# Performance work log

Measured on AMD Instinct MI355X. Metric: run time of the kernel, lower is better.

## Reference

```python
import jax, jax.numpy as jnp
import numpy as np


def setup_inputs() -> dict:
    key = jax.random.key(0)
    ks = jax.random.split(key, 6)
    B, S, D = 2, 2048, 1024
    E, DFF = 8, 2048  # E includes always-on expert 0; router sees E-1 routed experts
    scale = 0.02
    return {
        "hidden_states": jax.random.normal(ks[0], (B, S, D), dtype=jnp.float32),
        "router_w": jax.random.normal(ks[1], (D, E - 1), dtype=jnp.float32) * scale,
        "router_b": jnp.zeros((E - 1,), dtype=jnp.float32),
        "wg": jax.random.normal(ks[2], (E, D, DFF), dtype=jnp.float32) * scale,
        "wu": jax.random.normal(ks[3], (E, D, DFF), dtype=jnp.float32) * scale,
        "wd": jax.random.normal(ks[4], (E, DFF, D), dtype=jnp.float32) * scale,
        "top_k": 2,
    }


def _expert_mlp(x, wg_e, wu_e, wd_e):
    # SwiGLU MLP: down( silu(x @ gate) * (x @ up) )
    return (jax.nn.silu(x @ wg_e) * (x @ wu_e)) @ wd_e


def reference(hidden_states, router_w, router_b, wg, wu, wd, top_k):
    B, S, D = hidden_states.shape
    E = wg.shape[0]  # total experts incl. always-on expert 0
    x = hidden_states.reshape(-1, D)  # [T, D]
    T = x.shape[0]

    # Router over E-1 routed experts, softmax in float32
    router_logits = x @ router_w + router_b  # [T, E-1]
    probs = jax.nn.softmax(router_logits.astype(jnp.float32), axis=-1)
    topw, topi = jax.lax.top_k(probs, top_k)  # [T, k]
    topw = topw / jnp.sum(topw, axis=-1, keepdims=True)
    topw = topw.astype(x.dtype)

    # Dense combine weights over routed experts (0 for unselected)
    cw = jnp.zeros((T, E - 1), dtype=x.dtype)
    cw = cw.at[jnp.arange(T)[:, None], topi].add(topw)  # [T, E-1]

    # Always-on expert 0 with weight 1
    out = _expert_mlp(x, wg[0], wu[0], wd[0])  # [T, D]

    # Routed experts 1..E-1 (static small loop over experts)
    for e in range(1, E):
        ye = _expert_mlp(x, wg[e], wu[e], wd[e])  # [T, D]
        out = out + cw[:, e - 1, None] * ye

    return out.reshape(B, S, -1)
```

## Files before the change

### kernel.cpp

```cpp
#include <hip/hip_runtime.h>

#define T_TOK 4096
#define DIM   1024
#define DFF   2048
#define NE    8
#define NR    7
#define MAXNB 71
#define NY    (32 + MAXNB)
#define G_BUF 20480

typedef __bf16 bf16x8 __attribute__((ext_vector_type(8)));
typedef float  floatx4 __attribute__((ext_vector_type(4)));

__device__ __forceinline__ unsigned short f32_bf16(float f) {
  union { float f; unsigned int u; } v; v.f = f;
  unsigned int u = v.u;
  unsigned int r = (u + 0x7FFFu + ((u >> 16) & 1u)) >> 16;
  return (unsigned short)r;
}

typedef __attribute__((address_space(3))) void lds_void_t;
typedef const __attribute__((address_space(1))) void g_void_t;

__device__ __forceinline__ void gld16(const void* g, void* l) {
  __builtin_amdgcn_global_load_lds((g_void_t*)g, (lds_void_t*)l, 16, 0, 0);
}

__global__ __launch_bounds__(256) void cvt_x_kernel(const float4* __restrict__ in,
                                                    ushort4* __restrict__ out) {
  int i = blockIdx.x * 256 + threadIdx.x;
  float4 v = in[i];
  ushort4 o;
  o.x = f32_bf16(v.x); o.y = f32_bf16(v.y);
  o.z = f32_bf16(v.z); o.w = f32_bf16(v.w);
  out[i] = o;
}

__global__ __launch_bounds__(256) void router_kernel(const float* __restrict__ x,
                                                     const float* __restrict__ rw,
                                                     const float* __restrict__ rb,
                                                     int* __restrict__ idxR,
                                                     float* __restrict__ wslR,
                                                     int* __restrict__ cnt,
                                                     int4* __restrict__ tokE,
                                                     float2* __restrict__ tokW) {
  const int lane = threadIdx.x & 63;
  const int t = blockIdx.x * 4 + (threadIdx.x >> 6);
  const float* xr = x + (size_t)t * DIM;
  float acc[NR];
#pragma unroll
  for (int e = 0; e < NR; e++) acc[e] = 0.f;
  for (int d = lane; d < DIM; d += 64) {
    float xv = xr[d];
#pragma unroll
    for (int e = 0; e < NR; e++) acc[e] += xv * rw[d * NR + e];
  }
#pragma unroll
  for (int off = 32; off > 0; off >>= 1) {
#pragma unroll
    for (int e = 0; e < NR; e++) acc[e] += __shfl_xor(acc[e], off, 64);
  }
  if (lane == 0) {
    float lg[NR];
    float m = -1e30f;
#pragma unroll
    for (int e = 0; e < NR; e++) { lg[e] = acc[e] + rb[e]; m = fmaxf(m, lg[e]); }
    float p[NR], s = 0.f;
#pragma unroll
    for (int e = 0; e < NR; e++) { p[e] = expf(lg[e] - m); s += p[e]; }
#pragma unroll
    for (int e = 0; e < NR; e++) p[e] /= s;
    int i1 = 0;
#pragma unroll
    for (int e = 1; e < NR; e++) if (p[e] > p[i1]) i1 = e;
    int i2 = (i1 == 0) ? 1 : 0;
#pragma unroll
    for (int e = 0; e < NR; e++) if (e != i1 && p[e] > p[i2]) i2 = e;
    float w1 = p[i1], w2 = p[i2], sw = w1 + w2;
    float w1n = w1 / sw, w2n = w2 / sw;
    int s1 = atomicAdd(&cnt[i1], 1);
    idxR[i1 * 4096 + s1] = t; wslR[i1 * 4096 + s1] = w1n;
    int s2 = atomicAdd(&cnt[i2], 1);
    idxR[i2 * 4096 + s2] = t; wslR[i2 * 4096 + s2] = w2n;
    int4 te; te.x = i1; te.y = s1; te.z = i2; te.w = s2;
    tokE[t] = te;
    float2 tw; tw.x = w1n; tw.y = w2n;
    tokW[t] = tw;
  }
}

__global__ __launch_bounds__(256) void sched_kernel(const int* __restrict__ cnt,
                                                    int* __restrict__ idxR,
                                                    float* __restrict__ wslR,
                                                    int4* __restrict__ schedAll,
                                                    int4* __restrict__ schedP,
                                                    int* __restrict__ prefOut,
                                                    int rsb) {
  __shared__ int nb[NR], pref[NR];
  if (threadIdx.x == 0) {
    int p = 0;
    for (int e = 0; e < NR; e++) { int c = cnt[e]; int n = (c + 127) >> 7; nb[e] = n; pref[e] = p; p += n; }
  }
  __syncthreads();
  if (threadIdx.x < NR) prefOut[threadIdx.x] = pref[threadIdx.x];
  for (int e = 0; e < NR; e++) {
    int c = cnt[e], top = nb[e] * 128;
    for (int i = c + (int)threadIdx.x; i < top; i += 256) {
      idxR[e * 4096 + i] = 0; wslR[e * 4096 + i] = 0.f;
    }
  }
  const int NBtot = pref[NR - 1] + nb[NR - 1];
  for (int y = threadIdx.x; y < 32; y += 256) {
    int4 ent; ent.x = 0; ent.y = -1; ent.z = y * 128; ent.w = 0;
    schedAll[y] = ent;
  }
  for (int y = threadIdx.x; y < MAXNB; y += 256) {
    int4 ent; ent.x = -1; ent.y = 0; ent.z = 0; ent.w = 0;
    if (y < NBtot) {
#pragma unroll
      for (int e = 0; e < NR; e++)
        if (y >= pref[e] && y < pref[e] + nb[e]) {
          int rb2 = y - pref[e];
          ent.x = e + 1; ent.y = e * 4096 + rb2 * 128; ent.z = rsb + y * 128;
        }
    }
    schedAll[32 + y] = ent;
  }
  for (int i = threadIdx.x; i < NR * 32; i += 256) {
    int e = i >> 5, rb2 = i & 31;
    int4 ent; ent.w = 0;
    if (rb2 < nb[e]) { ent.x = e + 1; ent.y = e * 4096 + rb2 * 128; ent.z = rb2 * 128; }
    else             { ent.x = -1; ent.y = 0; ent.z = 0; }
    schedP[i] = ent;
  }
}

__global__ __launch_bounds__(256) void transpose_cvt_kernel(
    const float* __restrict__ wg, const float* __restrict__ wu, const float* __restrict__ wd,
    unsigned short* __restrict__ wgt, unsigned short* __restrict__ wut,
    unsigned short* __restrict__ wdt) {
  __shared__ float tile[64][65];
  const int z = blockIdx.z;
  const float* src; unsigned short* dst; int R, C;
  if (z < 8)       { src = wg + (size_t)z * DIM * DFF;        dst = wgt + (size_t)z * DIM * DFF;        R = DIM; C = DFF; }
  else if (z < 16) { src = wu + (size_t)(z - 8) * DIM * DFF;  dst = wut + (size_t)(z - 8) * DIM * DFF;  R = DIM; C = DFF; }
  else             { src = wd + (size_t)(z - 16) * DFF * DIM; dst = wdt + (size_t)(z - 16) * DFF * DIM; R = DFF; C = DIM; }
  const int c0 = blockIdx.x * 64, r0 = blockIdx.y * 64;
  if (c0 >= C || r0 >= R) return;
  const int tx = threadIdx.x & 63, ty = threadIdx.x >> 6;
#pragma unroll
  for (int j = ty; j < 64; j += 4)
    tile[j][tx] = src[(size_t)(r0 + j) * C + c0 + tx];
  __syncthreads();
  const int r2 = (threadIdx.x & 15) * 4, jj = threadIdx.x >> 4;
#pragma unroll
  for (int j = jj; j < 64; j += 16) {
    unsigned int lo = (unsigned int)f32_bf16(tile[r2 + 0][j]) | ((unsigned int)f32_bf16(tile[r2 + 1][j]) << 16);
    unsigned int hi = (unsigned int)f32_bf16(tile[r2 + 2][j]) | ((unsigned int)f32_bf16(tile[r2 + 3][j]) << 16);
    uint2 o; o.x = lo; o.y = hi;
    *(uint2*)(dst + (size_t)(c0 + j) * R + r0 + r2) = o;
  }
}

__global__ __launch_bounds__(512, 2) void gemm1_kernel(
    const unsigned short* __restrict__ xb, const unsigned short* __restrict__ wgt,
    const unsigned short* __restrict__ wut, const int* __restrict__ idxR,
    const int4* __restrict__ sched, unsigned short* __restrict__ h, int gy) {
  const int nblk = gridDim.x;
  int bid = blockIdx.x;
  { int q = nblk >> 3, r = nblk & 7, xc = bid & 7, p = bid >> 3;
    bid = (xc < r ? xc * (q + 1) : r * (q + 1) + (xc - r) * q) + p; }
  const int bx = bid / gy, by = bid - bx * gy;
  const int4 ent = sched[by];
  if (ent.x < 0) return;
  __shared__ unsigned short smem[3 * G_BUF];
  const int tid = threadIdx.x, lane = tid & 63, wid = tid >> 6;
  const int n0 = bx * 256;
  const int wm = (wid >> 2) * 64;
  const int wn = (wid & 3) * 64;
  const int fr = lane & 15, kq = lane >> 4;
  const int pl = (fr >> 1) * 64 + (((((fr & 1) << 2) | kq) ^ (fr >> 1)) << 3);
  int offA[4], offG[4], offU[4];
#pragma unroll
  for (int mi = 0; mi < 4; mi++) offA[mi] = (wm + mi * 16) * 32 + pl;
#pragma unroll
  for (int ni = 0; ni < 4; ni++) {
    offG[ni] = 4096 + (wn + ni * 16) * 32 + pl;
    offU[ni] = 12288 + (wn + ni * 16) * 32 + pl;
  }
  const int prA = tid >> 3;
  const int csA = (tid & 7) ^ (prA & 7);
  const int rowS = 2 * prA + (csA >> 2);
  const int colS = (csA & 3) * 8;
  int tokA;
  if (ent.y < 0) tokA = ent.z + rowS;
  else           tokA = idxR[ent.y + rowS];
  const unsigned short* wgt_e = wgt + (size_t)ent.x * DIM * DFF;
  const unsigned short* wut_e = wut + (size_t)ent.x * DIM * DFF;
  const unsigned short* gA  = xb + (size_t)tokA * DIM + colS;
  const unsigned short* gG0 = wgt_e + (size_t)(n0 + rowS) * DIM + colS;
  const unsigned short* gG1 = gG0 + (size_t)128 * DIM;
  const unsigned short* gU0 = wut_e + (size_t)(n0 + rowS) * DIM + colS;
  const unsigned short* gU1 = gU0 + (size_t)128 * DIM;
  floatx4 accg[4][4], accu[4][4];
  const floatx4 z4 = {0.f, 0.f, 0.f, 0.f};
#pragma unroll
  for (int i = 0; i < 4; i++)
#pragma unroll
    for (int j = 0; j < 4; j++) { accg[i][j] = z4; accu[i][j] = z4; }
  {
    unsigned short* d = smem + tid * 8;
    gld16(gA, d); gld16(gG0, d + 4096); gld16(gG1, d + 8192);
    gld16(gU0, d + 12288); gld16(gU1, d + 16384);
    unsigned short* e = smem + G_BUF + tid * 8;
    gld16(gA + 32, e); gld16(gG0 + 32, e + 4096); gld16(gG1 + 32, e + 8192);
    gld16(gU0 + 32, e + 12288); gld16(gU1 + 32, e + 16384);
  }
  asm volatile("s_waitcnt vmcnt(5)" ::: "memory");
  __builtin_amdgcn_s_barrier();
  int b = 0;
  for (int k = 0; k < 32; ++k) {
    const unsigned short* Bb = smem + b * G_BUF;
    int b2 = b + 2; if (b2 >= 3) b2 -= 3;
    unsigned short* db2 = smem + b2 * G_BUF + tid * 8;
    if (k < 30) {
      const int kt = (k + 2) * 32;
      gld16(gA + kt, db2); gld16(gG0 + kt, db2 + 4096); gld16(gG1 + kt, db2 + 8192);
      gld16(gU0 + kt, db2 + 12288); gld16(gU1 + kt, db2 + 16384);
    }
    __builtin_amdgcn_sched_barrier(0);
    bf16x8 a[4], g[4], u[4];
#pragma unroll
    for (int mi = 0; mi < 4; mi++) a[mi] = *(const bf16x8*)(Bb + offA[mi]);
#pragma unroll
    for (int ni = 0; ni < 4; ni++) {
      g[ni] = *(const bf16x8*)(Bb + offG[ni]);
      u[ni] = *(const bf16x8*)(Bb + offU[ni]);
    }
    __builtin_amdgcn_s_setprio(1);
#pragma unroll
    for (int mi = 0; mi < 4; mi++)
#pragma unroll
      for (int ni = 0; ni < 4; ni++)
        accg[mi][ni] = __builtin_amdgcn_mfma_f32_16x16x32_bf16(a[mi], g[ni], accg[mi][ni], 0, 0, 0);
#pragma unroll
    for (int mi = 0; mi < 4; mi++)
#pragma unroll
      for (int ni = 0; ni < 4; ni++)
        accu[mi][ni] = __builtin_amdgcn_mfma_f32_16x16x32_bf16(a[mi], u[ni], accu[mi][ni], 0, 0, 0);
    __builtin_amdgcn_s_setprio(0);
    __builtin_amdgcn_sched_barrier(0);
    if (k < 30)       asm volatile("s_waitcnt vmcnt(5)" ::: "memory");
    else if (k == 30) asm volatile("s_waitcnt vmcnt(0)" ::: "memory");
    __builtin_amdgcn_s_barrier();
    b++; if (b == 3) b = 0;
  }
  const int rb = kq * 4;
#pragma unroll
  for (int mi = 0; mi < 4; mi++)
#pragma unroll
    for (int ni = 0; ni < 4; ni++)
#pragma unroll
      for (int r = 0; r < 4; r++) {
        int row = ent.z + wm + mi * 16 + rb + r;
        int col = n0 + wn + ni * 16 + fr;
        float gv = accg[mi][ni][r], uv = accu[mi][ni][r];
        float hv = (gv / (1.f + __expf(-gv))) * uv;
        h[(size_t)row * DFF + col] = f32_bf16(hv);
      }
}

__global__ __launch_bounds__(512, 2) void gemm2_kernel(
    const unsigned short* __restrict__ hsrc, const unsigned short* __restrict__ wdt,
    const int4* __restrict__ sched, float* __restrict__ y, int gy) {
  const int nblk = gridDim.x;
  int bid = blockIdx.x;
  { int q = nblk >> 3, r = nblk & 7, xc = bid & 7, p = bid >> 3;
    bid = (xc < r ? xc * (q + 1) : r * (q + 1) + (xc - r) * q) + p; }
  const int bx = bid / gy, by = bid - bx * gy;
  const int4 ent = sched[by];
  if (ent.x < 0) return;
  __shared__ unsigned short smem[3 * G_BUF];
  const int tid = threadIdx.x, lane = tid & 63, wid = tid >> 6;
  const int n0 = bx * 512;
  const int wm = (wid >> 2) * 64;
  const int wn = (wid & 3) * 128;
  const int fr = lane & 15, kq = lane >> 4;
  const int pl = (fr >> 1) * 64 + (((((fr & 1) << 2) | kq) ^ (fr >> 1)) << 3);
  int offA[4], offB[8];
#pragma unroll
  for (int mi = 0; mi < 4; mi++) offA[mi] = (wm + mi * 16) * 32 + pl;
#pragma unroll
  for (int ni = 0; ni < 8; ni++) offB[ni] = 4096 + (wn + ni * 16) * 32 + pl;
  const int prA = tid >> 3;
  const int csA = (tid & 7) ^ (prA & 7);
  const int rowS = 2 * prA + (csA >> 2);
  const int colS = (csA & 3) * 8;
  const unsigned short* wdt_e = wdt + (size_t)ent.x * DFF * DIM;
  const unsigned short* gA  = hsrc + (size_t)(ent.z + rowS) * DFF + colS;
  const unsigned short* gB0 = wdt_e + (size_t)(n0 + rowS) * DFF + colS;
  const unsigned short* gB1 = gB0 + (size_t)128 * DFF;
  const unsigned short* gB2 = gB0 + (size_t)256 * DFF;
  const unsigned short* gB3 = gB0 + (size_t)384 * DFF;
  floatx4 acc[4][8];
  const floatx4 z4 = {0.f, 0.f, 0.f, 0.f};
#pragma unroll
  for (int i = 0; i < 4; i++)
#pragma unroll
    for (int j = 0; j < 8; j++) acc[i][j] = z4;
  {
    unsigned short* d = smem + tid * 8;
    gld16(gA, d); gld16(gB0, d + 4096); gld16(gB1, d + 8192);
    gld16(gB2, d + 12288); gld16(gB3, d + 16384);
    unsigned short* e = smem + G_BUF + tid * 8;
    gld16(gA + 32, e); gld16(gB0 + 32, e + 4096); gld16(gB1 + 32, e + 8192);
    gld16(gB2 + 32, e + 12288); gld16(gB3 + 32, e + 16384);
  }
  asm volatile("s_waitcnt vmcnt(5)" ::: "memory");
  __builtin_amdgcn_s_barrier();
  int b = 0;
  for (int k = 0; k < 64; ++k) {
    const unsigned short* Bb = smem + b * G_BUF;
    int b2 = b + 2; if (b2 >= 3) b2 -= 3;
    unsigned short* db2 = smem + b2 * G_BUF + tid * 8;
    if (k < 62) {
      const int kt = (k + 2) * 32;
      gld16(gA + kt, db2); gld16(gB0 + kt, db2 + 4096); gld16(gB1 + kt, db2 + 8192);
      gld16(gB2 + kt, db2 + 12288); gld16(gB3 + kt, db2 + 16384);
    }
    __builtin_amdgcn_sched_barrier(0);
    bf16x8 a[4], bf[8];
#pragma unroll
    for (int mi = 0; mi < 4; mi++) a[mi] = *(const bf16x8*)(Bb + offA[mi]);
#pragma unroll
    for (int ni = 0; ni < 8; ni++) bf[ni] = *(const bf16x8*)(Bb + offB[ni]);
    __builtin_amdgcn_s_setprio(1);
#pragma unroll
    for (int mi = 0; mi < 4; mi++)
#pragma unroll
      for (int ni = 0; ni < 8; ni++)
        acc[mi][ni] = __builtin_amdgcn_mfma_f32_16x16x32_bf16(a[mi], bf[ni], acc[mi][ni], 0, 0, 0);
    __builtin_amdgcn_s_setprio(0);
    __builtin_amdgcn_sched_barrier(0);
    if (k < 62)       asm volatile("s_waitcnt vmcnt(5)" ::: "memory");
    else if (k == 62) asm volatile("s_waitcnt vmcnt(0)" ::: "memory");
    __builtin_amdgcn_s_barrier();
    b++; if (b == 3) b = 0;
  }
  const int rb = kq * 4;
#pragma unroll
  for (int mi = 0; mi < 4; mi++)
#pragma unroll
    for (int ni = 0; ni < 8; ni++)
#pragma unroll
      for (int r = 0; r < 4; r++)
        y[(size_t)(ent.z + wm + mi * 16 + rb + r) * DIM + n0 + wn + ni * 16 + fr] = acc[mi][ni][r];
}

__global__ __launch_bounds__(256) void gemm2_atomic_kernel(
    const unsigned short* __restrict__ h, const unsigned short* __restrict__ wdt,
    const int* __restrict__ idxR, const float* __restrict__ wslR,
    const int4* __restrict__ sched, float* __restrict__ out) {
  const int4 ent = sched[blockIdx.y];
  if (ent.x < 0) return;
  __shared__ unsigned short As[128 * 32];
  __shared__ unsigned short Bs[128 * 32];
  const int tid = threadIdx.x, lane = tid & 63, wid = tid >> 6;
  const int n0 = blockIdx.x * 128;
  const int wm = (wid >> 1) * 64, wn = (wid & 1) * 64;
  floatx4 acc[4][4];
  const floatx4 z4 = {0.f, 0.f, 0.f, 0.f};
#pragma unroll
  for (int i = 0; i < 4; i++)
#pragma unroll
    for (int j = 0; j < 4; j++) acc[i][j] = z4;
  const unsigned short* wdt_e = wdt + (size_t)ent.x * DFF * DIM;
  const int srow = tid >> 2, scol = (tid & 3) * 8;
  const unsigned short* ap0 = h + (size_t)(ent.z + srow) * DFF + scol;
  const unsigned short* ap1 = ap0 + (size_t)64 * DFF;
  const unsigned short* bp0 = wdt_e + (size_t)(n0 + srow) * DFF + scol;
  const unsigned short* bp1 = bp0 + (size_t)64 * DFF;
  unsigned short* as0 = As + tid * 8;
  unsigned short* as1 = As + (256 + tid) * 8;
  unsigned short* bs0 = Bs + tid * 8;
  unsigned short* bs1 = Bs + (256 + tid) * 8;
  const int fr = lane & 15, kq = (lane >> 4) * 8;
  for (int k0 = 0; k0 < DFF; k0 += 32) {
    __syncthreads();
    gld16(ap0 + k0, as0); gld16(ap1 + k0, as1);
    gld16(bp0 + k0, bs0); gld16(bp1 + k0, bs1);
    __syncthreads();
    bf16x8 af[4], bf[4];
#pragma unroll
    for (int mi = 0; mi < 4; mi++) af[mi] = *(const bf16x8*)(As + (wm + mi * 16 + fr) * 32 + kq);
#pragma unroll
    for (int ni = 0; ni < 4; ni++) bf[ni] = *(const bf16x8*)(Bs + (wn + ni * 16 + fr) * 32 + kq);
#pragma unroll
    for (int mi = 0; mi < 4; mi++)
#pragma unroll
      for (int ni = 0; ni < 4; ni++)
        acc[mi][ni] = __builtin_amdgcn_mfma_f32_16x16x32_bf16(af[mi], bf[ni], acc[mi][ni], 0, 0, 0);
  }
  const int rb0 = wm + (lane >> 4) * 4;
  const int cb0 = n0 + wn + fr;
#pragma unroll
  for (int mi = 0; mi < 4; mi++)
#pragma unroll
    for (int r = 0; r < 4; r++) {
      int lrow = rb0 + mi * 16 + r;
      if (ent.y < 0) {
        int tok = ent.z + lrow;
#pragma unroll
        for (int ni = 0; ni < 4; ni++)
          out[(size_t)tok * DIM + cb0 + ni * 16] = acc[mi][ni][r];
      } else {
        int tok = idxR[ent.y + lrow];
        float s = wslR[ent.y + lrow];
        if (s != 0.f) {
#pragma unroll
          for (int ni = 0; ni < 4; ni++)
            atomicAdd(&out[(size_t)tok * DIM + cb0 + ni * 16], s * acc[mi][ni][r]);
        }
      }
    }
}

__global__ __launch_bounds__(256) void combine_kernel(const float* __restrict__ y,
                                                      const int4* __restrict__ tokE,
                                                      const float2* __restrict__ tokW,
                                                      const int* __restrict__ pref,
                                                      float* __restrict__ out) {
  const int t = blockIdx.x;
  const int c = threadIdx.x * 4;
  int4 te = tokE[t];
  float2 tw = tokW[t];
  int p1 = 4096 + pref[te.x] * 128 + te.y;
  int p2 = 4096 + pref[te.z] * 128 + te.w;
  float4 a = *(const float4*)(y + (size_t)t * DIM + c);
  float4 b = *(const float4*)(y + (size_t)p1 * DIM + c);
  float4 d = *(const float4*)(y + (size_t)p2 * DIM + c);
  float4 o;
  o.x = a.x + tw.x * b.x + tw.y * d.x;
  o.y = a.y + tw.x * b.y + tw.y * d.y;
  o.z = a.z + tw.x * b.z + tw.y * d.z;
  o.w = a.w + tw.x * b.w + tw.y * d.w;
  *(float4*)(out + (size_t)t * DIM + c) = o;
}

extern "C" void kernel_launch(void* const* d_in, const int* in_sizes, int n_in,
                              void* d_out, int out_size, void* d_ws, size_t ws_size,
                              hipStream_t stream) {
  const float* x  = (const float*)d_in[0];
  const float* rw = (const float*)d_in[1];
  const float* rb = (const float*)d_in[2];
  const float* wg = (const float*)d_in[3];
  const float* wu = (const float*)d_in[4];
  const float* wd = (const float*)d_in[5];
  float* out = (float*)d_out;

  const bool modeA = ws_size >= (size_t)163300000;
  const bool modeB = !modeA && ws_size >= (size_t)146700000;
  const size_t H_ROWS = modeA ? 13184 : (modeB ? 9088 : 4096);
  const int rsb = modeA ? 4096 : 0;

  char* p = (char*)d_ws;
  unsigned short* xb  = (unsigned short*)p; p += (size_t)T_TOK * DIM * 2;
  unsigned short* h   = (unsigned short*)p; p += H_ROWS * DFF * 2;
  unsigned short* wgt = (unsigned short*)p;
  float*          y   = (float*)p;          p += (size_t)NE * DIM * DFF * 2;
  unsigned short* wut = (unsigned short*)p; p += (size_t)NE * DIM * DFF * 2;
  unsigned short* wdt = (unsigned short*)p; p += (size_t)NE * DIM * DFF * 2;
  int*   idxR = (int*)p;   p += (size_t)NR * 4096 * 4;
  float* wslR;
  if (modeA) { wslR = (float*)wdt; }
  else       { wslR = (float*)p; p += (size_t)NR * 4096 * 4; }
  int*   cnt  = (int*)p;      p += 64;
  int*   pref = (int*)p;      p += 64;
  int4*  schedAll = (int4*)p; p += 2048;
  int4*  schedP   = (int4*)p; p += 4096;
  int4*  tokE = (int4*)p;     p += (size_t)T_TOK * 16;
  float2* tokW = (float2*)p;  p += (size_t)T_TOK * 8;

  cvt_x_kernel<<<dim3(T_TOK * DIM / 4 / 256), 256, 0, stream>>>((const float4*)x, (ushort4*)xb);
  hipMemsetAsync(cnt, 0, 64, stream);
  router_kernel<<<dim3(T_TOK / 4), 256, 0, stream>>>(x, rw, rb, idxR, wslR, cnt, tokE, tokW);
  sched_kernel<<<dim3(1), 256, 0, stream>>>(cnt, idxR, wslR, schedAll, schedP, pref, rsb);
  transpose_cvt_kernel<<<dim3(32, 32, 24), 256, 0, stream>>>(wg, wu, wd, wgt, wut, wdt);

  if (modeA) {
    gemm1_kernel<<<dim3((DFF / 256) * NY), 512, 0, stream>>>(xb, wgt, wut, idxR, schedAll, h, NY);
    gemm2_kernel<<<dim3((DIM / 512) * NY), 512, 0, stream>>>(h, wdt, schedAll, y, NY);
    combine_kernel<<<dim3(T_TOK), 256, 0, stream>>>(y, tokE, tokW, pref, out);
  } else if (modeB) {
    gemm1_kernel<<<dim3((DFF / 256) * 32), 512, 0, stream>>>(xb, wgt, wut, idxR, schedAll, h, 32);
    gemm2_atomic_kernel<<<dim3(DIM / 128, 32), 256, 0, stream>>>(h, wdt, idxR, wslR, schedAll, out);
    gemm1_kernel<<<dim3((DFF / 256) * MAXNB), 512, 0, stream>>>(xb, wgt, wut, idxR, schedAll + 32, h, MAXNB);
    gemm2_atomic_kernel<<<dim3(DIM / 128, MAXNB), 256, 0, stream>>>(h, wdt, idxR, wslR, schedAll + 32, out);
  } else {
    gemm1_kernel<<<dim3((DFF / 256) * 32), 512, 0, stream>>>(xb, wgt, wut, idxR, schedAll, h, 32);
    gemm2_atomic_kernel<<<dim3(DIM / 128, 32), 256, 0, stream>>>(h, wdt, idxR, wslR, schedAll, out);
    for (int e = 0; e < NR; e++) {
      gemm1_kernel<<<dim3((DFF / 256) * 32), 512, 0, stream>>>(xb, wgt, wut, idxR, schedP + e * 32, h, 32);
      gemm2_atomic_kernel<<<dim3(DIM / 128, 32), 256, 0, stream>>>(h, wdt, idxR, wslR, schedP + e * 32, out);
    }
  }
}
```

Baseline: 568.5 us.

## Re-tile grouped GEMMs into two-phase ping-pong with split gate/up warps

Both grouped GEMM kernels now give each warp the full 128-row M slice (8 MFMA row tiles) and a 64-wide N slice. In gemm1, the low four warps compute the gate product and the high four compute the up product, and the up accumulators are passed through LDS for the SiLU epilogue. Each K step is split into two halves, with barriers and global-load issue placed between the MFMA bursts, so that LDS reads, async copies and matrix math interleave across warps. The change adds barriers and an LDS exchange epilogue, and it changes register pressure, in exchange for less redundant LDS fragment traffic and better overlap.

```diff
diff --git a/kernel.cpp b/kernel.cpp
--- a/kernel.cpp
+++ b/kernel.cpp
@@ -176,18 +176,15 @@
   __shared__ unsigned short smem[3 * G_BUF];
   const int tid = threadIdx.x, lane = tid & 63, wid = tid >> 6;
   const int n0 = bx * 256;
-  const int wm = (wid >> 2) * 64;
   const int wn = (wid & 3) * 64;
   const int fr = lane & 15, kq = lane >> 4;
   const int pl = (fr >> 1) * 64 + (((((fr & 1) << 2) | kq) ^ (fr >> 1)) << 3);
-  int offA[4], offG[4], offU[4];
-#pragma unroll
-  for (int mi = 0; mi < 4; mi++) offA[mi] = (wm + mi * 16) * 32 + pl;
-#pragma unroll
-  for (int ni = 0; ni < 4; ni++) {
-    offG[ni] = 4096 + (wn + ni * 16) * 32 + pl;
-    offU[ni] = 12288 + (wn + ni * 16) * 32 + pl;
-  }
+  int offA[8], offB[4];
+#pragma unroll
+  for (int mi = 0; mi < 8; mi++) offA[mi] = mi * 512 + pl;
+  const int bsec = (wid < 4) ? 4096 : 12288;
+#pragma unroll
+  for (int ni = 0; ni < 4; ni++) offB[ni] = bsec + (wn + ni * 16) * 32 + pl;
   const int prA = tid >> 3;
   const int csA = (tid & 7) ^ (prA & 7);
   const int rowS = 2 * prA + (csA >> 2);
@@ -202,12 +199,12 @@
   const unsigned short* gG1 = gG0 + (size_t)128 * DIM;
   const unsigned short* gU0 = wut_e + (size_t)(n0 + rowS) * DIM + colS;
   const unsigned short* gU1 = gU0 + (size_t)128 * DIM;
-  floatx4 accg[4][4], accu[4][4];
+  floatx4 acc[8][4];
   const floatx4 z4 = {0.f, 0.f, 0.f, 0.f};
 #pragma unroll
-  for (int i = 0; i < 4; i++)
-#pragma unroll
-    for (int j = 0; j < 4; j++) { accg[i][j] = z4; accu[i][j] = z4; }
+  for (int i = 0; i < 8; i++)
+#pragma unroll
+    for (int j = 0; j < 4; j++) acc[i][j] = z4;
   {
     unsigned short* d = smem + tid * 8;
     gld16(gA, d); gld16(gG0, d + 4096); gld16(gG1, d + 8192);
@@ -219,55 +216,82 @@
   asm volatile("s_waitcnt vmcnt(5)" ::: "memory");
   __builtin_amdgcn_s_barrier();
   int b = 0;
+  bf16x8 a[8], bf[4];
   for (int k = 0; k < 32; ++k) {
     const unsigned short* Bb = smem + b * G_BUF;
     int b2 = b + 2; if (b2 >= 3) b2 -= 3;
     unsigned short* db2 = smem + b2 * G_BUF + tid * 8;
-    if (k < 30) {
-      const int kt = (k + 2) * 32;
-      gld16(gA + kt, db2); gld16(gG0 + kt, db2 + 4096); gld16(gG1 + kt, db2 + 8192);
-      gld16(gU0 + kt, db2 + 12288); gld16(gU1 + kt, db2 + 16384);
+    const bool pf = (k < 30);
+    const int kt = (k + 2) * 32;
+#pragma unroll
+    for (int mi = 0; mi < 4; mi++) a[mi] = *(const bf16x8*)(Bb + offA[mi]);
+#pragma unroll
+    for (int ni = 0; ni < 4; ni++) bf[ni] = *(const bf16x8*)(Bb + offB[ni]);
+    if (pf) { gld16(gA + kt, db2); gld16(gG0 + kt, db2 + 4096); gld16(gG1 + kt, db2 + 8192); }
+    __builtin_amdgcn_sched_barrier(0);
+    __builtin_amdgcn_s_barrier();
+    asm volatile("s_waitcnt lgkmcnt(0)" ::: "memory");
+    __builtin_amdgcn_sched_barrier(0);
+    __builtin_amdgcn_s_setprio(1);
+#pragma unroll
+    for (int mi = 0; mi < 4; mi++)
+#pragma unroll
+      for (int ni = 0; ni < 4; ni++)
+        acc[mi][ni] = __builtin_amdgcn_mfma_f32_16x16x32_bf16(a[mi], bf[ni], acc[mi][ni], 0, 0, 0);
+    __builtin_amdgcn_s_setprio(0);
+    __builtin_amdgcn_sched_barrier(0);
+    __builtin_amdgcn_s_barrier();
+#pragma unroll
+    for (int mi = 4; mi < 8; mi++) a[mi] = *(const bf16x8*)(Bb + offA[mi]);
+    if (pf) { gld16(gU0 + kt, db2 + 12288); gld16(gU1 + kt, db2 + 16384); }
+    __builtin_amdgcn_sched_barrier(0);
+    __builtin_amdgcn_s_barrier();
+    asm volatile("s_waitcnt lgkmcnt(0)" ::: "memory");
+    __builtin_amdgcn_sched_barrier(0);
+    __builtin_amdgcn_s_setprio(1);
+#pragma unroll
+    for (int mi = 4; mi < 8; mi++)
+#pragma unroll
+      for (int ni = 0; ni < 4; ni++)
+        acc[mi][ni] = __builtin_amdgcn_mfma_f32_16x16x32_bf16(a[mi], bf[ni], acc[mi][ni], 0, 0, 0);
+    __builtin_amdgcn_s_setprio(0);
+    __builtin_amdgcn_sched_barrier(0);
+    if (pf)           asm volatile("s_waitcnt vmcnt(5)" ::: "memory");
+    else if (k == 30) asm volatile("s_waitcnt vmcnt(0)" ::: "memory");
+    __builtin_amdgcn_s_barrier();
+    b++; if (b == 3) b = 0;
+  }
+  float* xch = (float*)smem;
+  const int xbase = (wid & 3) * (64 * 67) + lane * 67;
+#pragma unroll
+  for (int chunk = 0; chunk < 2; ++chunk) {
+    __syncthreads();
+    if (wid >= 4) {
+#pragma unroll
+      for (int mi = 0; mi < 4; mi++)
+#pragma unroll
+        for (int ni = 0; ni < 4; ni++)
+#pragma unroll
+          for (int r = 0; r < 4; r++)
+            xch[xbase + mi * 16 + ni * 4 + r] = acc[chunk * 4 + mi][ni][r];
     }
-    __builtin_amdgcn_sched_barrier(0);
-    bf16x8 a[4], g[4], u[4];
-#pragma unroll
-    for (int mi = 0; mi < 4; mi++) a[mi] = *(const bf16x8*)(Bb + offA[mi]);
-#pragma unroll
-    for (int ni = 0; ni < 4; ni++) {
-      g[ni] = *(const bf16x8*)(Bb + offG[ni]);
-      u[ni] = *(const bf16x8*)(Bb + offU[ni]);
+    __syncthreads();
+    if (wid < 4) {
+#pragma unroll
+      for (int mi = 0; mi < 4; mi++)
+#pragma unroll
+        for (int ni = 0; ni < 4; ni++)
+#pragma unroll
+          for (int r = 0; r < 4; r++) {
+            float gv = acc[chunk * 4 + mi][ni][r];
+            float uv = xch[xbase + mi * 16 + ni * 4 + r];
+            float hv = (gv / (1.f + __expf(-gv))) * uv;
+            int row = ent.z + (chunk * 4 + mi) * 16 + kq * 4 + r;
+            int col = n0 + wn + ni * 16 + fr;
+            h[(size_t)row * DFF + col] = f32_bf16(hv);
+          }
     }
-    __builtin_amdgcn_s_setprio(1);
-#pragma unroll
-    for (int mi = 0; mi < 4; mi++)
-#pragma unroll
-      for (int ni = 0; ni < 4; ni++)
-        accg[mi][ni] = __builtin_amdgcn_mfma_f32_16x16x32_bf16(a[mi], g[ni], accg[mi][ni], 0, 0, 0);
-#pragma unroll
-    for (int mi = 0; mi < 4; mi++)
-#pragma unroll
-      for (int ni = 0; ni < 4; ni++)
-        accu[mi][ni] = __builtin_amdgcn_mfma_f32_16x16x32_bf16(a[mi], u[ni], accu[mi][ni], 0, 0, 0);
-    __builtin_amdgcn_s_setprio(0);
-    __builtin_amdgcn_sched_barrier(0);
-    if (k < 30)       asm volatile("s_waitcnt vmcnt(5)" ::: "memory");
-    else if (k == 30) asm volatile("s_waitcnt vmcnt(0)" ::: "memory");
-    __builtin_amdgcn_s_barrier();
-    b++; if (b == 3) b = 0;
-  }
-  const int rb = kq * 4;
-#pragma unroll
-  for (int mi = 0; mi < 4; mi++)
-#pragma unroll
-    for (int ni = 0; ni < 4; ni++)
-#pragma unroll
-      for (int r = 0; r < 4; r++) {
-        int row = ent.z + wm + mi * 16 + rb + r;
-        int col = n0 + wn + ni * 16 + fr;
-        float gv = accg[mi][ni][r], uv = accu[mi][ni][r];
-        float hv = (gv / (1.f + __expf(-gv))) * uv;
-        h[(size_t)row * DFF + col] = f32_bf16(hv);
-      }
+  }
 }
 
 __global__ __launch_bounds__(512, 2) void gemm2_kernel(
@@ -283,15 +307,14 @@
   __shared__ unsigned short smem[3 * G_BUF];
   const int tid = threadIdx.x, lane = tid & 63, wid = tid >> 6;
   const int n0 = bx * 512;
-  const int wm = (wid >> 2) * 64;
-  const int wn = (wid & 3) * 128;
+  const int wn = wid * 64;
   const int fr = lane & 15, kq = lane >> 4;
   const int pl = (fr >> 1) * 64 + (((((fr & 1) << 2) | kq) ^ (fr >> 1)) << 3);
-  int offA[4], offB[8];
-#pragma unroll
-  for (int mi = 0; mi < 4; mi++) offA[mi] = (wm + mi * 16) * 32 + pl;
-#pragma unroll
-  for (int ni = 0; ni < 8; ni++) offB[ni] = 4096 + (wn + ni * 16) * 32 + pl;
+  int offA[8], offB[4];
+#pragma unroll
+  for (int mi = 0; mi < 8; mi++) offA[mi] = mi * 512 + pl;
+#pragma unroll
+  for (int ni = 0; ni < 4; ni++) offB[ni] = 4096 + (wn + ni * 16) * 32 + pl;
   const int prA = tid >> 3;
   const int csA = (tid & 7) ^ (prA & 7);
   const int rowS = 2 * prA + (csA >> 2);
@@ -302,12 +325,12 @@
   const unsigned short* gB1 = gB0 + (size_t)128 * DFF;
   const unsigned short* gB2 = gB0 + (size_t)256 * DFF;
   const unsigned short* gB3 = gB0 + (size_t)384 * DFF;
-  floatx4 acc[4][8];
+  floatx4 acc[8][4];
   const floatx4 z4 = {0.f, 0.f, 0.f, 0.f};
 #pragma unroll
-  for (int i = 0; i < 4; i++)
-#pragma unroll
-    for (int j = 0; j < 8; j++) acc[i][j] = z4;
+  for (int i = 0; i < 8; i++)
+#pragma unroll
+    for (int j = 0; j < 4; j++) acc[i][j] = z4;
   {
     unsigned short* d = smem + tid * 8;
     gld16(gA, d); gld16(gB0, d + 4096); gld16(gB1, d + 8192);
@@ -319,42 +342,59 @@
   asm volatile("s_waitcnt vmcnt(5)" ::: "memory");
   __builtin_amdgcn_s_barrier();
   int b = 0;
+  bf16x8 a[8], bf[4];
   for (int k = 0; k < 64; ++k) {
     const unsigned short* Bb = smem + b * G_BUF;
     int b2 = b + 2; if (b2 >= 3) b2 -= 3;
     unsigned short* db2 = smem + b2 * G_BUF + tid * 8;
-    if (k < 62) {
-      const int kt = (k + 2) * 32;
-      gld16(gA + kt, db2); gld16(gB0 + kt, db2 + 4096); gld16(gB1 + kt, db2 + 8192);
-      gld16(gB2 + kt, db2 + 12288); gld16(gB3 + kt, db2 + 16384);
-    }
-    __builtin_amdgcn_sched_barrier(0);
-    bf16x8 a[4], bf[8];
+    const bool pf = (k < 62);
+    const int kt = (k + 2) * 32;
 #pragma unroll
     for (int mi = 0; mi < 4; mi++) a[mi] = *(const bf16x8*)(Bb + offA[mi]);
 #pragma unroll
-    for (int ni = 0; ni < 8; ni++) bf[ni] = *(const bf16x8*)(Bb + offB[ni]);
+    for (int ni = 0; ni < 4; ni++) bf[ni] = *(const bf16x8*)(Bb + offB[ni]);
+    if (pf) { gld16(gA + kt, db2); gld16(gB0 + kt, db2 + 4096); gld16(gB1 + kt, db2 + 8192); }
+    __builtin_amdgcn_sched_barrier(0);
+    __builtin_amdgcn_s_barrier();
+    asm volatile("s_waitcnt lgkmcnt(0)" ::: "memory");
+    __builtin_amdgcn_sched_barrier(0);
     __builtin_amdgcn_s_setprio(1);
 #pragma unroll
     for (int mi = 0; mi < 4; mi++)
 #pragma unroll
-      for (int ni = 0; ni < 8; ni++)
+      for (int ni = 0; ni < 4; ni++)
         acc[mi][ni] = __builtin_amdgcn_mfma_f32_16x16x32_bf16(a[mi], bf[ni], acc[mi][ni], 0, 0, 0);
     __builtin_amdgcn_s_setprio(0);
     __builtin_amdgcn_sched_barrier(0);
-    if (k < 62)       asm volatile("s_waitcnt vmcnt(5)" ::: "memory");
+    __builtin_amdgcn_s_barrier();
+#pragma unroll
+    for (int mi = 4; mi < 8; mi++) a[mi] = *(const bf16x8*)(Bb + offA[mi]);
+    if (pf) { gld16(gB2 + kt, db2 + 12288); gld16(gB3 + kt, db2 + 16384); }
+    __builtin_amdgcn_sched_barrier(0);
+    __builtin_amdgcn_s_barrier();
+    asm volatile("s_waitcnt lgkmcnt(0)" ::: "memory");
+    __builtin_amdgcn_sched_barrier(0);
+    __builtin_amdgcn_s_setprio(1);
+#pragma unroll
+    for (int mi = 4; mi < 8; mi++)
+#pragma unroll
+      for (int ni = 0; ni < 4; ni++)
+        acc[mi][ni] = __builtin_amdgcn_mfma_f32_16x16x32_bf16(a[mi], bf[ni], acc[mi][ni], 0, 0, 0);
+    __builtin_amdgcn_s_setprio(0);
+    __builtin_amdgcn_sched_barrier(0);
+    if (pf)           asm volatile("s_waitcnt vmcnt(5)" ::: "memory");
     else if (k == 62) asm volatile("s_waitcnt vmcnt(0)" ::: "memory");
     __builtin_amdgcn_s_barrier();
     b++; if (b == 3) b = 0;
   }
   const int rb = kq * 4;
 #pragma unroll
-  for (int mi = 0; mi < 4; mi++)
-#pragma unroll
-    for (int ni = 0; ni < 8; ni++)
+  for (int mi = 0; mi < 8; mi++)
+#pragma unroll
+    for (int ni = 0; ni < 4; ni++)
 #pragma unroll
       for (int r = 0; r < 4; r++)
-        y[(size_t)(ent.z + wm + mi * 16 + rb + r) * DIM + n0 + wn + ni * 16 + fr] = acc[mi][ni][r];
+        y[(size_t)(ent.z + mi * 16 + rb + r) * DIM + n0 + wn + ni * 16 + fr] = acc[mi][ni][r];
 }
 
 __global__ __launch_bounds__(256) void gemm2_atomic_kernel(
@@ -390,16 +430,16 @@
     gld16(ap0 + k0, as0); gld16(ap1 + k0, as1);
     gld16(bp0 + k0, bs0); gld16(bp1 + k0, bs1);
     __syncthreads();
-    bf16x8 af[4], bf[4];
+    bf16x8 af[4], bfv[4];
 #pragma unroll
     for (int mi = 0; mi < 4; mi++) af[mi] = *(const bf16x8*)(As + (wm + mi * 16 + fr) * 32 + kq);
 #pragma unroll
-    for (int ni = 0; ni < 4; ni++) bf[ni] = *(const bf16x8*)(Bs + (wn + ni * 16 + fr) * 32 + kq);
+    for (int ni = 0; ni < 4; ni++) bfv[ni] = *(const bf16x8*)(Bs + (wn + ni * 16 + fr) * 32 + kq);
 #pragma unroll
     for (int mi = 0; mi < 4; mi++)
 #pragma unroll
       for (int ni = 0; ni < 4; ni++)
-        acc[mi][ni] = __builtin_amdgcn_mfma_f32_16x16x32_bf16(af[mi], bf[ni], acc[mi][ni], 0, 0, 0);
+        acc[mi][ni] = __builtin_amdgcn_mfma_f32_16x16x32_bf16(af[mi], bfv[ni], acc[mi][ni], 0, 0, 0);
   }
   const int rb0 = wm + (lane >> 4) * 4;
   const int cb0 = n0 + wn + fr;
```

New measurement: 577.5 us. Within noise of the previous version (+1.6%).

## Load A operand directly to registers and split gate/up across wave groups

Applied to the files above, without the earlier changes.

Both GEMM kernels stop staging the A tile (activations) through LDS and instead load each wave's A fragments straight from global memory into registers, double-buffered across k-steps. In gemm1 the warp layout changes so half the waves compute the gate projection and half the up projection over a wider N tile, with the results exchanged through LDS in the epilogue to apply SiLU·up. This cuts LDS footprint and LDS read traffic per k-step, but makes A loads redundant across waves (served from cache) and adds an LDS exchange plus barriers in the gemm1 epilogue.

```diff
diff --git a/kernel.cpp b/kernel.cpp
--- a/kernel.cpp
+++ b/kernel.cpp
@@ -7,7 +7,7 @@
 #define NR    7
 #define MAXNB 71
 #define NY    (32 + MAXNB)
-#define G_BUF 20480
+#define BUFU  16384
 
 typedef __bf16 bf16x8 __attribute__((ext_vector_type(8)));
 typedef float  floatx4 __attribute__((ext_vector_type(4)));
@@ -162,6 +162,40 @@
   }
 }
 
+#define G1_TILE(KX, CUR, NXT)                                                            \
+  {                                                                                      \
+    const int k_ = (KX);                                                                 \
+    if (k_ < 31) {                                                                       \
+      _Pragma("unroll")                                                                  \
+      for (int mi = 0; mi < 4; mi++)                                                     \
+        NXT[mi] = *(const bf16x8*)(aP[mi] + (k_ + 1) * 32);                              \
+    }                                                                                    \
+    __builtin_amdgcn_sched_barrier(0);                                                   \
+    if (k_ < 30) {                                                                       \
+      const int kt_ = (k_ + 2) * 32;                                                     \
+      unsigned short* d_ = smem + b2_ * BUFU + tid * 8;                                  \
+      gld16(gG0 + kt_, d_);        gld16(gG1 + kt_, d_ + 4096);                          \
+      gld16(gU0 + kt_, d_ + 8192); gld16(gU1 + kt_, d_ + 12288);                         \
+    }                                                                                    \
+    __builtin_amdgcn_sched_barrier(0);                                                   \
+    const unsigned short* Bb_ = smem + b_ * BUFU + secB;                                 \
+    bf16x8 bf[8];                                                                        \
+    _Pragma("unroll")                                                                    \
+    for (int nb = 0; nb < 8; nb++) bf[nb] = *(const bf16x8*)(Bb_ + offB[nb]);            \
+    __builtin_amdgcn_s_setprio(1);                                                       \
+    _Pragma("unroll")                                                                    \
+    for (int mi = 0; mi < 4; mi++)                                                       \
+      _Pragma("unroll")                                                                  \
+      for (int nb = 0; nb < 8; nb++)                                                     \
+        acc[mi][nb] = __builtin_amdgcn_mfma_f32_16x16x32_bf16(CUR[mi], bf[nb], acc[mi][nb], 0, 0, 0); \
+    __builtin_amdgcn_s_setprio(0);                                                       \
+    __builtin_amdgcn_sched_barrier(0);                                                   \
+    if (k_ < 30)       asm volatile("s_waitcnt vmcnt(4)" ::: "memory");                  \
+    else if (k_ == 30) asm volatile("s_waitcnt vmcnt(0)" ::: "memory");                  \
+    __builtin_amdgcn_s_barrier();                                                        \
+    b_ = (b_ == 2) ? 0 : b_ + 1;  b2_ = (b2_ == 2) ? 0 : b2_ + 1;                        \
+  }
+
 __global__ __launch_bounds__(512, 2) void gemm1_kernel(
     const unsigned short* __restrict__ xb, const unsigned short* __restrict__ wgt,
     const unsigned short* __restrict__ wut, const int* __restrict__ idxR,
@@ -173,102 +207,127 @@
   const int bx = bid / gy, by = bid - bx * gy;
   const int4 ent = sched[by];
   if (ent.x < 0) return;
-  __shared__ unsigned short smem[3 * G_BUF];
+  __shared__ unsigned short smem[3 * BUFU];
   const int tid = threadIdx.x, lane = tid & 63, wid = tid >> 6;
   const int n0 = bx * 256;
-  const int wm = (wid >> 2) * 64;
-  const int wn = (wid & 3) * 64;
+  const int wm = (wid & 1) * 64;
+  const int wn = ((wid >> 1) & 1) * 128;
+  const bool isU = (wid >= 4);
+  const int secB = isU ? 8192 : 0;
   const int fr = lane & 15, kq = lane >> 4;
   const int pl = (fr >> 1) * 64 + (((((fr & 1) << 2) | kq) ^ (fr >> 1)) << 3);
-  int offA[4], offG[4], offU[4];
-#pragma unroll
-  for (int mi = 0; mi < 4; mi++) offA[mi] = (wm + mi * 16) * 32 + pl;
-#pragma unroll
-  for (int ni = 0; ni < 4; ni++) {
-    offG[ni] = 4096 + (wn + ni * 16) * 32 + pl;
-    offU[ni] = 12288 + (wn + ni * 16) * 32 + pl;
-  }
-  const int prA = tid >> 3;
-  const int csA = (tid & 7) ^ (prA & 7);
-  const int rowS = 2 * prA + (csA >> 2);
-  const int colS = (csA & 3) * 8;
-  int tokA;
-  if (ent.y < 0) tokA = ent.z + rowS;
-  else           tokA = idxR[ent.y + rowS];
+  int offB[8];
+#pragma unroll
+  for (int nb = 0; nb < 8; nb++) offB[nb] = (wn + nb * 16) * 32 + pl;
+  const unsigned short* aP[4];
+#pragma unroll
+  for (int mi = 0; mi < 4; mi++) {
+    int row = wm + mi * 16 + fr;
+    int tok = (ent.y < 0) ? (ent.z + row) : idxR[ent.y + row];
+    aP[mi] = xb + (size_t)tok * DIM + kq * 8;
+  }
+  const int pr = tid >> 3;
+  const int cs = (tid & 7) ^ (pr & 7);
+  const int rowS = 2 * pr + (cs >> 2);
+  const int colS = (cs & 3) * 8;
   const unsigned short* wgt_e = wgt + (size_t)ent.x * DIM * DFF;
   const unsigned short* wut_e = wut + (size_t)ent.x * DIM * DFF;
-  const unsigned short* gA  = xb + (size_t)tokA * DIM + colS;
   const unsigned short* gG0 = wgt_e + (size_t)(n0 + rowS) * DIM + colS;
   const unsigned short* gG1 = gG0 + (size_t)128 * DIM;
   const unsigned short* gU0 = wut_e + (size_t)(n0 + rowS) * DIM + colS;
   const unsigned short* gU1 = gU0 + (size_t)128 * DIM;
-  floatx4 accg[4][4], accu[4][4];
+  floatx4 acc[4][8];
   const floatx4 z4 = {0.f, 0.f, 0.f, 0.f};
 #pragma unroll
   for (int i = 0; i < 4; i++)
 #pragma unroll
-    for (int j = 0; j < 4; j++) { accg[i][j] = z4; accu[i][j] = z4; }
+    for (int j = 0; j < 8; j++) acc[i][j] = z4;
+  bf16x8 areg0[4], areg1[4];
   {
+#pragma unroll
+    for (int mi = 0; mi < 4; mi++) areg0[mi] = *(const bf16x8*)(aP[mi]);
+    __builtin_amdgcn_sched_barrier(0);
     unsigned short* d = smem + tid * 8;
-    gld16(gA, d); gld16(gG0, d + 4096); gld16(gG1, d + 8192);
-    gld16(gU0, d + 12288); gld16(gU1, d + 16384);
-    unsigned short* e = smem + G_BUF + tid * 8;
-    gld16(gA + 32, e); gld16(gG0 + 32, e + 4096); gld16(gG1 + 32, e + 8192);
-    gld16(gU0 + 32, e + 12288); gld16(gU1 + 32, e + 16384);
-  }
-  asm volatile("s_waitcnt vmcnt(5)" ::: "memory");
-  __builtin_amdgcn_s_barrier();
-  int b = 0;
-  for (int k = 0; k < 32; ++k) {
-    const unsigned short* Bb = smem + b * G_BUF;
-    int b2 = b + 2; if (b2 >= 3) b2 -= 3;
-    unsigned short* db2 = smem + b2 * G_BUF + tid * 8;
-    if (k < 30) {
-      const int kt = (k + 2) * 32;
-      gld16(gA + kt, db2); gld16(gG0 + kt, db2 + 4096); gld16(gG1 + kt, db2 + 8192);
-      gld16(gU0 + kt, db2 + 12288); gld16(gU1 + kt, db2 + 16384);
+    gld16(gG0, d);        gld16(gG1, d + 4096);
+    gld16(gU0, d + 8192); gld16(gU1, d + 12288);
+    unsigned short* e = smem + BUFU + tid * 8;
+    gld16(gG0 + 32, e);        gld16(gG1 + 32, e + 4096);
+    gld16(gU0 + 32, e + 8192); gld16(gU1 + 32, e + 12288);
+    __builtin_amdgcn_sched_barrier(0);
+    asm volatile("s_waitcnt vmcnt(4)" ::: "memory");
+    __builtin_amdgcn_s_barrier();
+  }
+  int b_ = 0, b2_ = 2;
+  for (int k0 = 0; k0 < 32; k0 += 2) {
+    G1_TILE(k0,     areg0, areg1);
+    G1_TILE(k0 + 1, areg1, areg0);
+  }
+  float* xch = (float*)smem;
+  const int xbase = (wid & 3) * (64 * 65) + lane * 65;
+#pragma unroll
+  for (int c = 0; c < 2; ++c) {
+    __syncthreads();
+    if (isU) {
+#pragma unroll
+      for (int mi = 0; mi < 4; mi++)
+#pragma unroll
+        for (int nq = 0; nq < 4; nq++)
+#pragma unroll
+          for (int r = 0; r < 4; r++)
+            xch[xbase + mi * 16 + nq * 4 + r] = acc[mi][c * 4 + nq][r];
     }
-    __builtin_amdgcn_sched_barrier(0);
-    bf16x8 a[4], g[4], u[4];
-#pragma unroll
-    for (int mi = 0; mi < 4; mi++) a[mi] = *(const bf16x8*)(Bb + offA[mi]);
-#pragma unroll
-    for (int ni = 0; ni < 4; ni++) {
-      g[ni] = *(const bf16x8*)(Bb + offG[ni]);
-      u[ni] = *(const bf16x8*)(Bb + offU[ni]);
+    __syncthreads();
+    if (!isU) {
+#pragma unroll
+      for (int mi = 0; mi < 4; mi++)
+#pragma unroll
+        for (int nq = 0; nq < 4; nq++)
+#pragma unroll
+          for (int r = 0; r < 4; r++) {
+            float gv = acc[mi][c * 4 + nq][r];
+            float uv = xch[xbase + mi * 16 + nq * 4 + r];
+            float hv = (gv / (1.f + __expf(-gv))) * uv;
+            int row = ent.z + wm + mi * 16 + kq * 4 + r;
+            int col = n0 + wn + (c * 4 + nq) * 16 + fr;
+            h[(size_t)row * DFF + col] = f32_bf16(hv);
+          }
     }
-    __builtin_amdgcn_s_setprio(1);
-#pragma unroll
-    for (int mi = 0; mi < 4; mi++)
-#pragma unroll
-      for (int ni = 0; ni < 4; ni++)
-        accg[mi][ni] = __builtin_amdgcn_mfma_f32_16x16x32_bf16(a[mi], g[ni], accg[mi][ni], 0, 0, 0);
-#pragma unroll
-    for (int mi = 0; mi < 4; mi++)
-#pragma unroll
-      for (int ni = 0; ni < 4; ni++)
-        accu[mi][ni] = __builtin_amdgcn_mfma_f32_16x16x32_bf16(a[mi], u[ni], accu[mi][ni], 0, 0, 0);
-    __builtin_amdgcn_s_setprio(0);
-    __builtin_amdgcn_sched_barrier(0);
-    if (k < 30)       asm volatile("s_waitcnt vmcnt(5)" ::: "memory");
-    else if (k == 30) asm volatile("s_waitcnt vmcnt(0)" ::: "memory");
-    __builtin_amdgcn_s_barrier();
-    b++; if (b == 3) b = 0;
-  }
-  const int rb = kq * 4;
-#pragma unroll
-  for (int mi = 0; mi < 4; mi++)
-#pragma unroll
-    for (int ni = 0; ni < 4; ni++)
-#pragma unroll
-      for (int r = 0; r < 4; r++) {
-        int row = ent.z + wm + mi * 16 + rb + r;
-        int col = n0 + wn + ni * 16 + fr;
-        float gv = accg[mi][ni][r], uv = accu[mi][ni][r];
-        float hv = (gv / (1.f + __expf(-gv))) * uv;
-        h[(size_t)row * DFF + col] = f32_bf16(hv);
-      }
-}
+  }
+}
+
+#define G2_TILE(KX, CUR, NXT)                                                            \
+  {                                                                                      \
+    const int k_ = (KX);                                                                 \
+    if (k_ < 63) {                                                                       \
+      _Pragma("unroll")                                                                  \
+      for (int mi = 0; mi < 4; mi++)                                                     \
+        NXT[mi] = *(const bf16x8*)(aP[mi] + (k_ + 1) * 32);                              \
+    }                                                                                    \
+    __builtin_amdgcn_sched_barrier(0);                                                   \
+    if (k_ < 62) {                                                                       \
+      const int kt_ = (k_ + 2) * 32;                                                     \
+      unsigned short* d_ = smem + b2_ * BUFU + tid * 8;                                  \
+      gld16(gB0 + kt_, d_);        gld16(gB1 + kt_, d_ + 4096);                          \
+      gld16(gB2 + kt_, d_ + 8192); gld16(gB3 + kt_, d_ + 12288);                         \
+    }                                                                                    \
+    __builtin_amdgcn_sched_barrier(0);                                                   \
+    const unsigned short* Bb_ = smem + b_ * BUFU;                                        \
+    bf16x8 bf[8];                                                                        \
+    _Pragma("unroll")                                                                    \
+    for (int nb = 0; nb < 8; nb++) bf[nb] = *(const bf16x8*)(Bb_ + offB[nb]);            \
+    __builtin_amdgcn_s_setprio(1);                                                       \
+    _Pragma("unroll")                                                                    \
+    for (int mi = 0; mi < 4; mi++)                                                       \
+      _Pragma("unroll")                                                                  \
+      for (int nb = 0; nb < 8; nb++)                                                     \
+        acc[mi][nb] = __builtin_amdgcn_mfma_f32_16x16x32_bf16(CUR[mi], bf[nb], acc[mi][nb], 0, 0, 0); \
+    __builtin_amdgcn_s_setprio(0);                                                       \
+    __builtin_amdgcn_sched_barrier(0);                                                   \
+    if (k_ < 62)       asm volatile("s_waitcnt vmcnt(4)" ::: "memory");                  \
+    else if (k_ == 62) asm volatile("s_waitcnt vmcnt(0)" ::: "memory");                  \
+    __builtin_amdgcn_s_barrier();                                                        \
+    b_ = (b_ == 2) ? 0 : b_ + 1;  b2_ = (b2_ == 2) ? 0 : b2_ + 1;                        \
+  }
 
 __global__ __launch_bounds__(512, 2) void gemm2_kernel(
     const unsigned short* __restrict__ hsrc, const unsigned short* __restrict__ wdt,
@@ -280,24 +339,27 @@
   const int bx = bid / gy, by = bid - bx * gy;
   const int4 ent = sched[by];
   if (ent.x < 0) return;
-  __shared__ unsigned short smem[3 * G_BUF];
+  __shared__ unsigned short smem[3 * BUFU];
   const int tid = threadIdx.x, lane = tid & 63, wid = tid >> 6;
   const int n0 = bx * 512;
-  const int wm = (wid >> 2) * 64;
-  const int wn = (wid & 3) * 128;
+  const int wm = (wid & 1) * 64;
+  const int wn = (wid >> 1) * 128;
   const int fr = lane & 15, kq = lane >> 4;
   const int pl = (fr >> 1) * 64 + (((((fr & 1) << 2) | kq) ^ (fr >> 1)) << 3);
-  int offA[4], offB[8];
-#pragma unroll
-  for (int mi = 0; mi < 4; mi++) offA[mi] = (wm + mi * 16) * 32 + pl;
-#pragma unroll
-  for (int ni = 0; ni < 8; ni++) offB[ni] = 4096 + (wn + ni * 16) * 32 + pl;
-  const int prA = tid >> 3;
-  const int csA = (tid & 7) ^ (prA & 7);
-  const int rowS = 2 * prA + (csA >> 2);
-  const int colS = (csA & 3) * 8;
+  int offB[8];
+#pragma unroll
+  for (int nb = 0; nb < 8; nb++) offB[nb] = (wn + nb * 16) * 32 + pl;
+  const unsigned short* aP[4];
+#pragma unroll
+  for (int mi = 0; mi < 4; mi++) {
+    int row = ent.z + wm + mi * 16 + fr;
+    aP[mi] = hsrc + (size_t)row * DFF + kq * 8;
+  }
+  const int pr = tid >> 3;
+  const int cs = (tid & 7) ^ (pr & 7);
+  const int rowS = 2 * pr + (cs >> 2);
+  const int colS = (cs & 3) * 8;
   const unsigned short* wdt_e = wdt + (size_t)ent.x * DFF * DIM;
-  const unsigned short* gA  = hsrc + (size_t)(ent.z + rowS) * DFF + colS;
   const unsigned short* gB0 = wdt_e + (size_t)(n0 + rowS) * DFF + colS;
   const unsigned short* gB1 = gB0 + (size_t)128 * DFF;
   const unsigned short* gB2 = gB0 + (size_t)256 * DFF;
@@ -308,53 +370,34 @@
   for (int i = 0; i < 4; i++)
 #pragma unroll
     for (int j = 0; j < 8; j++) acc[i][j] = z4;
+  bf16x8 areg0[4], areg1[4];
   {
+#pragma unroll
+    for (int mi = 0; mi < 4; mi++) areg0[mi] = *(const bf16x8*)(aP[mi]);
+    __builtin_amdgcn_sched_barrier(0);
     unsigned short* d = smem + tid * 8;
-    gld16(gA, d); gld16(gB0, d + 4096); gld16(gB1, d + 8192);
-    gld16(gB2, d + 12288); gld16(gB3, d + 16384);
-    unsigned short* e = smem + G_BUF + tid * 8;
-    gld16(gA + 32, e); gld16(gB0 + 32, e + 4096); gld16(gB1 + 32, e + 8192);
-    gld16(gB2 + 32, e + 12288); gld16(gB3 + 32, e + 16384);
-  }
-  asm volatile("s_waitcnt vmcnt(5)" ::: "memory");
-  __builtin_amdgcn_s_barrier();
-  int b = 0;
-  for (int k = 0; k < 64; ++k) {
-    const unsigned short* Bb = smem + b * G_BUF;
-    int b2 = b + 2; if (b2 >= 3) b2 -= 3;
-    unsigned short* db2 = smem + b2 * G_BUF + tid * 8;
-    if (k < 62) {
-      const int kt = (k + 2) * 32;
-      gld16(gA + kt, db2); gld16(gB0 + kt, db2 + 4096); gld16(gB1 + kt, db2 + 8192);
-      gld16(gB2 + kt, db2 + 12288); gld16(gB3 + kt, db2 + 16384);
-    }
+    gld16(gB0, d);        gld16(gB1, d + 4096);
+    gld16(gB2, d + 8192); gld16(gB3, d + 12288);
+    unsigned short* e = smem + BUFU + tid * 8;
+    gld16(gB0 + 32, e);        gld16(gB1 + 32, e + 4096);
+    gld16(gB2 + 32, e + 8192); gld16(gB3 + 32, e + 12288);
     __builtin_amdgcn_sched_barrier(0);
-    bf16x8 a[4], bf[8];
-#pragma unroll
-    for (int mi = 0; mi < 4; mi++) a[mi] = *(const bf16x8*)(Bb + offA[mi]);
-#pragma unroll
-    for (int ni = 0; ni < 8; ni++) bf[ni] = *(const bf16x8*)(Bb + offB[ni]);
-    __builtin_amdgcn_s_setprio(1);
-#pragma unroll
-    for (int mi = 0; mi < 4; mi++)
-#pragma unroll
-      for (int ni = 0; ni < 8; ni++)
-        acc[mi][ni] = __builtin_amdgcn_mfma_f32_16x16x32_bf16(a[mi], bf[ni], acc[mi][ni], 0, 0, 0);
-    __builtin_amdgcn_s_setprio(0);
-    __builtin_amdgcn_sched_barrier(0);
-    if (k < 62)       asm volatile("s_waitcnt vmcnt(5)" ::: "memory");
-    else if (k == 62) asm volatile("s_waitcnt vmcnt(0)" ::: "memory");
+    asm volatile("s_waitcnt vmcnt(4)" ::: "memory");
     __builtin_amdgcn_s_barrier();
-    b++; if (b == 3) b = 0;
+  }
+  int b_ = 0, b2_ = 2;
+  for (int k0 = 0; k0 < 64; k0 += 2) {
+    G2_TILE(k0,     areg0, areg1);
+    G2_TILE(k0 + 1, areg1, areg0);
   }
   const int rb = kq * 4;
 #pragma unroll
   for (int mi = 0; mi < 4; mi++)
 #pragma unroll
-    for (int ni = 0; ni < 8; ni++)
+    for (int nb = 0; nb < 8; nb++)
 #pragma unroll
       for (int r = 0; r < 4; r++)
-        y[(size_t)(ent.z + wm + mi * 16 + rb + r) * DIM + n0 + wn + ni * 16 + fr] = acc[mi][ni][r];
+        y[(size_t)(ent.z + wm + mi * 16 + rb + r) * DIM + n0 + wn + nb * 16 + fr] = acc[mi][nb][r];
 }
 
 __global__ __launch_bounds__(256) void gemm2_atomic_kernel(
@@ -390,16 +433,16 @@
     gld16(ap0 + k0, as0); gld16(ap1 + k0, as1);
     gld16(bp0 + k0, bs0); gld16(bp1 + k0, bs1);
     __syncthreads();
-    bf16x8 af[4], bf[4];
+    bf16x8 af[4], bfv[4];
 #pragma unroll
     for (int mi = 0; mi < 4; mi++) af[mi] = *(const bf16x8*)(As + (wm + mi * 16 + fr) * 32 + kq);
 #pragma unroll
-    for (int ni = 0; ni < 4; ni++) bf[ni] = *(const bf16x8*)(Bs + (wn + ni * 16 + fr) * 32 + kq);
+    for (int ni = 0; ni < 4; ni++) bfv[ni] = *(const bf16x8*)(Bs + (wn + ni * 16 + fr) * 32 + kq);
 #pragma unroll
     for (int mi = 0; mi < 4; mi++)
 #pragma unroll
       for (int ni = 0; ni < 4; ni++)
-        acc[mi][ni] = __builtin_amdgcn_mfma_f32_16x16x32_bf16(af[mi], bf[ni], acc[mi][ni], 0, 0, 0);
+        acc[mi][ni] = __builtin_amdgcn_mfma_f32_16x16x32_bf16(af[mi], bfv[ni], acc[mi][ni], 0, 0, 0);
   }
   const int rb0 = wm + (lane >> 4) * 4;
   const int cb0 = n0 + wn + fr;
```

Measured after the change: 696.6 us. 1.23x slower.
